# Kernel optimization log

Measured on AMD Instinct MI355X. Metric: run time of the kernel, lower is better.

## Reference

```python
import math
import jax, jax.numpy as jnp
import numpy as np

EPS = 1e-12
NHEAD = 12
HEAD_DIM = 64  # d_model // nhead = 768 // 12


def setup_inputs() -> dict:
    key = jax.random.key(0)
    ks = jax.random.split(key, 8)
    L, D, H = 12, 768, 2048
    B, S = 8, 1024
    std = 0.02
    return {
        "x": jax.random.normal(ks[0], (B, S, D), jnp.float32),
        "wq": jax.random.normal(ks[1], (L, D, D), jnp.float32) * std,
        "wk": jax.random.normal(ks[2], (L, D, D), jnp.float32) * std,
        "wv": jax.random.normal(ks[3], (L, D, D), jnp.float32) * std,
        "wo": jax.random.normal(ks[4], (L, D, D), jnp.float32) * std,
        "w1": jax.random.normal(ks[5], (L, H, D), jnp.float32) * std,
        "w2": jax.random.normal(ks[6], (L, D, H), jnp.float32) * std,
        "attn_norm_w": jnp.ones((L, D), jnp.float32),
        "ffn_norm_w": jnp.ones((L, D), jnp.float32),
    }


def _rmsnorm(x, w):
    # x * rsqrt(mean(x^2) + eps) * w
    return x * jax.lax.rsqrt(jnp.mean(x * x, axis=-1, keepdims=True) + EPS) * w


def _block(x, params):
    wq, wk, wv, wo, w1, w2, anw, fnw = params
    B, S, D = x.shape
    # --- attention (manual matmul-softmax-matmul, fp32 softmax) ---
    xn = _rmsnorm(x, anw)
    q = jnp.einsum('bsd,ed->bse', xn, wq).reshape(B, S, NHEAD, HEAD_DIM)
    k = jnp.einsum('bsd,ed->bse', xn, wk).reshape(B, S, NHEAD, HEAD_DIM)
    v = jnp.einsum('bsd,ed->bse', xn, wv).reshape(B, S, NHEAD, HEAD_DIM)
    scores = jnp.einsum('bqhd,bkhd->bhqk', q, k) / math.sqrt(HEAD_DIM)
    probs = jax.nn.softmax(scores.astype(jnp.float32), axis=-1).astype(x.dtype)
    attn = jnp.einsum('bhqk,bkhd->bqhd', probs, v).reshape(B, S, D)
    h = x + jnp.einsum('bsd,ed->bse', attn, wo)
    # --- FFN: w2(silu(w1(h_norm))) ---
    hn = _rmsnorm(h, fnw)
    ff = jnp.einsum('bsh,dh->bsd', jax.nn.silu(jnp.einsum('bsd,hd->bsh', hn, w1)), w2)
    return h + ff


def reference(x, wq, wk, wv, wo, w1, w2, attn_norm_w, ffn_norm_w):
    def step(carry, p):
        return _block(carry, p), None
    out, _ = jax.lax.scan(step, x, (wq, wk, wv, wo, w1, w2, attn_norm_w, ffn_norm_w))
    return out
```

## Files before the change

kernel.cpp:

```cpp
#include <hip/hip_runtime.h>
#include <stdint.h>

typedef unsigned short u16;
typedef unsigned int u32;
typedef __bf16 bf16x8 __attribute__((ext_vector_type(8)));
typedef __bf16 bf16x4 __attribute__((ext_vector_type(4)));
typedef float f32x4 __attribute__((ext_vector_type(4)));

__device__ __forceinline__ u16 f2bf(float f) {
  u32 u = __builtin_bit_cast(u32, f);
  u32 r = (u + 0x7FFFu + ((u >> 16) & 1u)) >> 16;
  return (u16)r;
}

__global__ __launch_bounds__(256)
void convert_w(const float* __restrict__ wq, const float* __restrict__ wk,
               const float* __restrict__ wv, const float* __restrict__ wo,
               const float* __restrict__ w1, const float* __restrict__ w2,
               u16* __restrict__ out) {
  size_t i = ((size_t)blockIdx.x * 256 + threadIdx.x) * 4;
  if (i >= 5505024) return;
  const float* src; size_t off;
  if (i < 589824)       { src = wq; off = i; }
  else if (i < 1179648) { src = wk; off = i - 589824; }
  else if (i < 1769472) { src = wv; off = i - 1179648; }
  else if (i < 2359296) { src = wo; off = i - 1769472; }
  else if (i < 3932160) { src = w1; off = i - 2359296; }
  else                  { src = w2; off = i - 3932160; }
  float4 v = *(const float4*)(src + off);
  u32 lo = (u32)f2bf(v.x) | ((u32)f2bf(v.y) << 16);
  u32 hi = (u32)f2bf(v.z) | ((u32)f2bf(v.w) << 16);
  *(uint2*)(out + i) = make_uint2(lo, hi);
}

__device__ __forceinline__ void rn_store4(u16* p, float4 v, float4 w, float sc) {
  u32 lo = (u32)f2bf(v.x * sc * w.x) | ((u32)f2bf(v.y * sc * w.y) << 16);
  u32 hi = (u32)f2bf(v.z * sc * w.z) | ((u32)f2bf(v.w * sc * w.w) << 16);
  *(uint2*)p = make_uint2(lo, hi);
}

__global__ __launch_bounds__(256)
void rmsnorm_k(const float* __restrict__ x, const float* __restrict__ w,
               u16* __restrict__ out) {
  const int tok = (blockIdx.x << 2) + (threadIdx.x >> 6);
  const int l = threadIdx.x & 63;
  const float* xr = x + (size_t)tok * 768;
  float4 v0 = *(const float4*)(xr + l * 4);
  float4 v1 = *(const float4*)(xr + 256 + l * 4);
  float4 v2 = *(const float4*)(xr + 512 + l * 4);
  float ss = v0.x*v0.x + v0.y*v0.y + v0.z*v0.z + v0.w*v0.w
           + v1.x*v1.x + v1.y*v1.y + v1.z*v1.z + v1.w*v1.w
           + v2.x*v2.x + v2.y*v2.y + v2.z*v2.z + v2.w*v2.w;
  ss += __shfl_xor(ss, 1);  ss += __shfl_xor(ss, 2);  ss += __shfl_xor(ss, 4);
  ss += __shfl_xor(ss, 8);  ss += __shfl_xor(ss, 16); ss += __shfl_xor(ss, 32);
  float sc = rsqrtf(ss * (1.f / 768.f) + 1e-12f);
  float4 w0 = *(const float4*)(w + l * 4);
  float4 w1v = *(const float4*)(w + 256 + l * 4);
  float4 w2v = *(const float4*)(w + 512 + l * 4);
  u16* o = out + (size_t)tok * 768;
  rn_store4(o + l * 4, v0, w0, sc);
  rn_store4(o + 256 + l * 4, v1, w1v, sc);
  rn_store4(o + 512 + l * 4, v2, w2v, sc);
}

#define GEMM_CORE(A_, W_, K_, m0_, n0_)                                             \
  for (int kt = 0; kt < (K_); kt += 64) {                                           \
    __syncthreads();                                                                \
    _Pragma("unroll")                                                               \
    for (int ii = 0; ii < 4; ++ii) {                                                \
      int issue = (w << 2) + ii;                                                    \
      int r = (issue << 3) + (l >> 3);                                              \
      int c = (l & 7) ^ (r & 7);                                                    \
      __builtin_amdgcn_global_load_lds((A_) + (size_t)((m0_) + r) * (K_) + kt + c * 8, \
                                       As + issue * 512, 16, 0, 0);                 \
      __builtin_amdgcn_global_load_lds((W_) + (size_t)((n0_) + r) * (K_) + kt + c * 8, \
                                       Ws + issue * 512, 16, 0, 0);                 \
    }                                                                               \
    __syncthreads();                                                                \
    _Pragma("unroll")                                                               \
    for (int kc = 0; kc < 2; ++kc) {                                                \
      int chunk = lg + (kc << 2);                                                   \
      bf16x8 af[4], bfr[4];                                                         \
      _Pragma("unroll")                                                             \
      for (int i = 0; i < 4; ++i) {                                                 \
        int mr = (wm << 6) + (i << 4) + ll;                                         \
        af[i] = *(const bf16x8*)((const char*)As + mr * 128 + ((chunk ^ (mr & 7)) << 4)); \
        int nr = (wn << 6) + (i << 4) + ll;                                         \
        bfr[i] = *(const bf16x8*)((const char*)Ws + nr * 128 + ((chunk ^ (nr & 7)) << 4)); \
      }                                                                             \
      _Pragma("unroll")                                                             \
      for (int i = 0; i < 4; ++i)                                                   \
        _Pragma("unroll")                                                           \
        for (int j = 0; j < 4; ++j)                                                 \
          acc[i][j] = __builtin_amdgcn_mfma_f32_16x16x32_bf16(af[i], bfr[j], acc[i][j], 0, 0, 0); \
    }                                                                               \
  }

template<int EP>
__global__ __launch_bounds__(256, 2)
void gemm_bt(const u16* __restrict__ A, const u16* __restrict__ W,
             void* __restrict__ outp, const float* __restrict__ Res,
             int M, int N, int K) {
  __shared__ __align__(16) u16 As[128 * 64];
  __shared__ __align__(16) u16 Ws[128 * 64];
  const int tid = threadIdx.x;
  const int w = tid >> 6, l = tid & 63;
  const int lg = l >> 4, ll = l & 15;
  const int ntiles = N >> 7;
  const int mt = blockIdx.x / ntiles, nt = blockIdx.x - mt * ntiles;
  const int m0 = mt << 7, n0 = nt << 7;
  const int wm = w >> 1, wn = w & 1;

  const f32x4 fz = {0.f, 0.f, 0.f, 0.f};
  f32x4 acc[4][4];
#pragma unroll
  for (int i = 0; i < 4; ++i)
#pragma unroll
    for (int j = 0; j < 4; ++j) acc[i][j] = fz;

  GEMM_CORE(A, W, K, m0, n0)

  const int g4 = lg << 2;
#pragma unroll
  for (int i = 0; i < 4; ++i) {
#pragma unroll
    for (int j = 0; j < 4; ++j) {
      int row0 = m0 + (wm << 6) + (i << 4) + g4;
      int col = n0 + (wn << 6) + (j << 4) + ll;
      f32x4 v = acc[i][j];
      if (EP == 0) {
        u16* o = (u16*)outp;
#pragma unroll
        for (int e = 0; e < 4; ++e) o[(size_t)(row0 + e) * N + col] = f2bf(v[e]);
      } else if (EP == 1) {
        float* o = (float*)outp;
#pragma unroll
        for (int e = 0; e < 4; ++e) {
          size_t idx = (size_t)(row0 + e) * N + col;
          o[idx] = Res[idx] + v[e];
        }
      } else {
        u16* o = (u16*)outp;
#pragma unroll
        for (int e = 0; e < 4; ++e) {
          float xx = v[e];
          o[(size_t)(row0 + e) * N + col] = f2bf(xx / (1.f + __expf(-xx)));
        }
      }
    }
  }
}

__global__ __launch_bounds__(256, 4)
void gemm_bt64(const u16* __restrict__ A, const u16* __restrict__ W,
               float* __restrict__ outp, const float* __restrict__ Res,
               int M, int N, int K) {
  __shared__ __align__(16) u16 As[64 * 64];
  __shared__ __align__(16) u16 Ws[128 * 64];
  const int tid = threadIdx.x;
  const int w = tid >> 6, l = tid & 63;
  const int lg = l >> 4, ll = l & 15;
  const int ntiles = N >> 7;
  const int mt = blockIdx.x / ntiles, nt = blockIdx.x - mt * ntiles;
  const int m0 = mt << 6, n0 = nt << 7;
  const int wm = w >> 1, wn = w & 1;

  const f32x4 fz = {0.f, 0.f, 0.f, 0.f};
  f32x4 acc[2][4];
#pragma unroll
  for (int i = 0; i < 2; ++i)
#pragma unroll
    for (int j = 0; j < 4; ++j) acc[i][j] = fz;

  for (int kt = 0; kt < K; kt += 64) {
    __syncthreads();
#pragma unroll
    for (int ii = 0; ii < 6; ++ii) {
      int issue = w * 6 + ii;
      if (issue < 8) {
        int r = (issue << 3) + (l >> 3);
        int c = (l & 7) ^ (r & 7);
        __builtin_amdgcn_global_load_lds(A + (size_t)(m0 + r) * K + kt + c * 8,
                                         As + issue * 512, 16, 0, 0);
      } else {
        int is2 = issue - 8;
        int r = (is2 << 3) + (l >> 3);
        int c = (l & 7) ^ (r & 7);
        __builtin_amdgcn_global_load_lds(W + (size_t)(n0 + r) * K + kt + c * 8,
                                         Ws + is2 * 512, 16, 0, 0);
      }
    }
    __syncthreads();
#pragma unroll
    for (int kc = 0; kc < 2; ++kc) {
      int chunk = lg + (kc << 2);
      bf16x8 af[2], bfr[4];
#pragma unroll
      for (int i = 0; i < 2; ++i) {
        int mr = (wm << 5) + (i << 4) + ll;
        af[i] = *(const bf16x8*)((const char*)As + mr * 128 + ((chunk ^ (mr & 7)) << 4));
      }
#pragma unroll
      for (int j = 0; j < 4; ++j) {
        int nr = (wn << 6) + (j << 4) + ll;
        bfr[j] = *(const bf16x8*)((const char*)Ws + nr * 128 + ((chunk ^ (nr & 7)) << 4));
      }
#pragma unroll
      for (int i = 0; i < 2; ++i)
#pragma unroll
        for (int j = 0; j < 4; ++j)
          acc[i][j] = __builtin_amdgcn_mfma_f32_16x16x32_bf16(af[i], bfr[j], acc[i][j], 0, 0, 0);
    }
  }

  const int g4 = lg << 2;
#pragma unroll
  for (int i = 0; i < 2; ++i) {
#pragma unroll
    for (int j = 0; j < 4; ++j) {
      int row0 = m0 + (wm << 5) + (i << 4) + g4;
      int col = n0 + (wn << 6) + (j << 4) + ll;
      f32x4 v = acc[i][j];
#pragma unroll
      for (int e = 0; e < 4; ++e) {
        size_t idx = (size_t)(row0 + e) * N + col;
        outp[idx] = Res[idx] + v[e];
      }
    }
  }
}

__global__ __launch_bounds__(256, 2)
void gemm_qkv(const u16* __restrict__ A, const u16* __restrict__ W,
              u16* __restrict__ Qo, u16* __restrict__ Ko, u16* __restrict__ Vo) {
  __shared__ __align__(16) u16 As[128 * 64];
  __shared__ __align__(16) u16 Ws[128 * 64];
  const int tid = threadIdx.x;
  const int w = tid >> 6, l = tid & 63;
  const int lg = l >> 4, ll = l & 15;
  const int mt = blockIdx.x / 18, nt = blockIdx.x - mt * 18;
  const int m0 = mt << 7, n0 = nt << 7;
  const int wm = w >> 1, wn = w & 1;
  const int K = 768;

  const f32x4 fz = {0.f, 0.f, 0.f, 0.f};
  f32x4 acc[4][4];
#pragma unroll
  for (int i = 0; i < 4; ++i)
#pragma unroll
    for (int j = 0; j < 4; ++j) acc[i][j] = fz;

  GEMM_CORE(A, W, K, m0, n0)

  const int g4 = lg << 2;
#pragma unroll
  for (int i = 0; i < 4; ++i) {
#pragma unroll
    for (int j = 0; j < 4; ++j) {
      int row0 = m0 + (wm << 6) + (i << 4) + g4;
      int col = n0 + (wn << 6) + (j << 4) + ll;
      f32x4 v = acc[i][j];
      if (nt < 12) {
        u16* o = (nt < 6) ? Qo : Ko;
        int c = (nt < 6) ? col : (col - 768);
#pragma unroll
        for (int e = 0; e < 4; ++e) o[(size_t)(row0 + e) * 768 + c] = f2bf(v[e]);
      } else {
        int c = col - 1536;
        int vrow = ((row0 >> 10) * 768) + c;
        u32 lo = (u32)f2bf(v[0]) | ((u32)f2bf(v[1]) << 16);
        u32 hi = (u32)f2bf(v[2]) | ((u32)f2bf(v[3]) << 16);
        *(uint2*)(Vo + ((size_t)vrow << 10) + (row0 & 1023)) = make_uint2(lo, hi);
      }
    }
  }
}

__global__ __launch_bounds__(256, 2)
void attn_kernel(const u16* __restrict__ Q, const u16* __restrict__ Kg,
                 const u16* __restrict__ Vt, u16* __restrict__ Og) {
  __shared__ __align__(16) __bf16 Ks[128 * 64];
  __shared__ __align__(16) __bf16 Vs[64 * 128];
  __shared__ __align__(16) __bf16 Ps[4][16 * 128];

  const int tid = threadIdx.x;
  const int w = tid >> 6, l = tid & 63;
  const int lg = l >> 4, ll = l & 15;
  const int bid = blockIdx.x;
  const int qt = bid / 96;
  const int bh = bid - qt * 96;
  const int b = bh / 12, hh = bh - b * 12;
  const float SC = 0.125f * 1.44269504f;

  bf16x8 qf[2][2];
  {
    const int tq = (b << 10) + (qt << 7) + (w << 5);
#pragma unroll
    for (int fm = 0; fm < 2; ++fm)
#pragma unroll
      for (int kc = 0; kc < 2; ++kc)
        qf[fm][kc] = *(const bf16x8*)(Q + (size_t)(tq + fm * 16 + ll) * 768 + hh * 64 + kc * 32 + lg * 8);
  }

  bf16x8 kp[4], vp[4];
#define ISSUE_KV(t_)                                                                  \
  { _Pragma("unroll")                                                                 \
    for (int ii = 0; ii < 4; ++ii) {                                                  \
      int issue = (w << 2) + ii;                                                      \
      int r = (issue << 3) + (l >> 3);                                                \
      int c = (l & 7) ^ (r & 7);                                                      \
      kp[ii] = *(const bf16x8*)(Kg + (size_t)((b << 10) + ((t_) << 7) + r) * 768 + hh * 64 + c * 8); \
      int rv = (issue << 2) + (l >> 4);                                               \
      int cv = ll ^ (rv & 7);                                                         \
      vp[ii] = *(const bf16x8*)(Vt + (size_t)((bh << 6) + rv) * 1024 + ((t_) << 7) + cv * 8); \
    } }
#define WRITE_KV                                                                      \
  { _Pragma("unroll")                                                                 \
    for (int ii = 0; ii < 4; ++ii) {                                                  \
      int issue = (w << 2) + ii;                                                      \
      *(bf16x8*)((char*)Ks + issue * 1024 + l * 16) = kp[ii];                         \
      *(bf16x8*)((char*)Vs + issue * 1024 + l * 16) = vp[ii];                         \
    } }

  const f32x4 fz = {0.f, 0.f, 0.f, 0.f};
  f32x4 oacc[4][2];
#pragma unroll
  for (int i = 0; i < 4; ++i) { oacc[i][0] = fz; oacc[i][1] = fz; }
  float mrow2[2] = {-1e30f, -1e30f};
  float lrow2[2] = {0.f, 0.f};

  ISSUE_KV(0);
  WRITE_KV;
  __syncthreads();

  for (int kt = 0; kt < 8; ++kt) {
    if (kt < 7) ISSUE_KV(kt + 1);

    f32x4 sa[2][8];
#pragma unroll
    for (int fm = 0; fm < 2; ++fm)
#pragma unroll
      for (int fn = 0; fn < 8; ++fn) sa[fm][fn] = fz;
    __builtin_amdgcn_s_setprio(1);
#pragma unroll
    for (int kc = 0; kc < 2; ++kc) {
      int chunk = lg + (kc << 2);
      bf16x8 kb[8];
#pragma unroll
      for (int fn = 0; fn < 8; ++fn) {
        int nr = (fn << 4) + ll;
        kb[fn] = *(const bf16x8*)((const char*)Ks + nr * 128 + ((chunk ^ (nr & 7)) << 4));
      }
#pragma unroll
      for (int fm = 0; fm < 2; ++fm)
#pragma unroll
        for (int fn = 0; fn < 8; ++fn)
          sa[fm][fn] = __builtin_amdgcn_mfma_f32_16x16x32_bf16(kb[fn], qf[fm][kc], sa[fm][fn], 0, 0, 0);
    }
    __builtin_amdgcn_s_setprio(0);

#pragma unroll
    for (int fm = 0; fm < 2; ++fm) {
      f32x4 vm = sa[fm][0];
#pragma unroll
      for (int fn = 1; fn < 8; ++fn) {
#pragma unroll
        for (int e = 0; e < 4; ++e) vm[e] = fmaxf(vm[e], sa[fm][fn][e]);
      }
      float mx = fmaxf(fmaxf(vm[0], vm[1]), fmaxf(vm[2], vm[3]));
      mx = fmaxf(mx, __shfl_xor(mx, 16));
      mx = fmaxf(mx, __shfl_xor(mx, 32));
      float mnew = fmaxf(mrow2[fm], mx);
      float c2 = mnew * SC;
      float scal = __builtin_amdgcn_exp2f(__builtin_fmaf(SC, mrow2[fm], -c2));

      f32x4 vsum = fz;
#pragma unroll
      for (int fn = 0; fn < 8; ++fn) {
        f32x4 p;
#pragma unroll
        for (int e = 0; e < 4; ++e)
          p[e] = __builtin_amdgcn_exp2f(__builtin_fmaf(SC, sa[fm][fn][e], -c2));
        vsum += p;
        bf16x4 pv4;
#pragma unroll
        for (int e = 0; e < 4; ++e) pv4[e] = (__bf16)p[e];
        int chunk = (fn << 1) + (lg >> 1);
        *(bf16x4*)((char*)&Ps[w][0] + ll * 256 + ((chunk ^ (ll & 7)) << 4) + ((lg & 1) << 3)) = pv4;
      }
      float rs = (vsum[0] + vsum[1]) + (vsum[2] + vsum[3]);
      rs += __shfl_xor(rs, 16);
      rs += __shfl_xor(rs, 32);
      lrow2[fm] = lrow2[fm] * scal + rs;
      mrow2[fm] = mnew;

      asm volatile("" ::: "memory");

#pragma unroll
      for (int fd = 0; fd < 4; ++fd) oacc[fd][fm] *= scal;

      __builtin_amdgcn_s_setprio(1);
#pragma unroll
      for (int ch = 0; ch < 4; ++ch) {
        int chunk = lg + (ch << 2);
        int qr = ll;
        bf16x8 pb = *(const bf16x8*)((const char*)&Ps[w][0] + qr * 256 + ((chunk ^ (qr & 7)) << 4));
#pragma unroll
        for (int fd = 0; fd < 4; ++fd) {
          int dr = (fd << 4) + ll;
          bf16x8 av = *(const bf16x8*)((const char*)Vs + dr * 256 + ((chunk ^ (dr & 7)) << 4));
          oacc[fd][fm] = __builtin_amdgcn_mfma_f32_16x16x32_bf16(av, pb, oacc[fd][fm], 0, 0, 0);
        }
      }
      __builtin_amdgcn_s_setprio(0);

      asm volatile("" ::: "memory");
    }

    if (kt < 7) {
      __syncthreads();
      WRITE_KV;
      __syncthreads();
    }
  }
#undef ISSUE_KV
#undef WRITE_KV

  float inv0 = 1.f / lrow2[0];
  float inv1 = 1.f / lrow2[1];
  const int tq0 = (b << 10) + (qt << 7) + (w << 5);
#pragma unroll
  for (int fd = 0; fd < 4; ++fd) {
#pragma unroll
    for (int fo = 0; fo < 2; ++fo) {
      int q = (fo << 4) + ll;
      float inv = fo ? inv1 : inv0;
      f32x4 v = oacc[fd][fo];
      int d0 = (fd << 4) + (lg << 2);
      u16* o = Og + (size_t)(tq0 + q) * 768 + hh * 64 + d0;
      u32 lo = (u32)f2bf(v[0] * inv) | ((u32)f2bf(v[1] * inv) << 16);
      u32 hi = (u32)f2bf(v[2] * inv) | ((u32)f2bf(v[3] * inv) << 16);
      *(uint2*)o = make_uint2(lo, hi);
    }
  }
}

extern "C" void kernel_launch(void* const* d_in, const int* in_sizes, int n_in,
                              void* d_out, int out_size, void* d_ws, size_t ws_size,
                              hipStream_t stream) {
  const float* x = (const float*)d_in[0];
  const float* wq = (const float*)d_in[1];
  const float* wk = (const float*)d_in[2];
  const float* wv = (const float*)d_in[3];
  const float* wo = (const float*)d_in[4];
  const float* w1 = (const float*)d_in[5];
  const float* w2 = (const float*)d_in[6];
  const float* anw = (const float*)d_in[7];
  const float* fnw = (const float*)d_in[8];

  char* ws = (char*)d_ws;
  float* h    = (float*)(ws);
  u16* xn     = (u16*)(ws + 25165824);
  u16* qb     = (u16*)(ws + 37748736);
  u16* kb     = (u16*)(ws + 50331648);
  u16* vt     = (u16*)(ws + 62914560);
  u16* ff1    = (u16*)(ws + 75497472);
  u16* wbuf   = (u16*)(ws + 109051904);

  hipMemcpyAsync(h, x, 25165824, hipMemcpyDeviceToDevice, stream);

  for (int L = 0; L < 12; ++L) {
    convert_w<<<5376, 256, 0, stream>>>(
        wq + (size_t)L * 589824, wk + (size_t)L * 589824,
        wv + (size_t)L * 589824, wo + (size_t)L * 589824,
        w1 + (size_t)L * 1572864, w2 + (size_t)L * 1572864, wbuf);
    rmsnorm_k<<<2048, 256, 0, stream>>>(h, anw + L * 768, xn);
    gemm_qkv<<<1152, 256, 0, stream>>>(xn, wbuf, qb, kb, vt);
    attn_kernel<<<768, 256, 0, stream>>>(qb, kb, vt, qb);
    gemm_bt64<<<768, 256, 0, stream>>>(qb, wbuf + 1769472, h, h, 8192, 768, 768);
    rmsnorm_k<<<2048, 256, 0, stream>>>(h, fnw + L * 768, xn);
    gemm_bt<2><<<1024, 256, 0, stream>>>(xn, wbuf + 2359296, ff1, nullptr, 8192, 2048, 768);
    float* outw = (L == 11) ? (float*)d_out : h;
    gemm_bt64<<<768, 256, 0, stream>>>(ff1, wbuf + 3932160, outw, h, 8192, 768, 2048);
  }
}
```

Measured before the change: 2.646 ms.

## Halve attention query tile per block and alias probability buffer onto K tile

The attention kernel now handles 64 query rows per block, 16 per wave, and launches twice as many blocks. The separate shared-memory buffer for softmax probabilities is removed; each wave writes its probabilities into its slice of the K tile, with an added barrier after the QK product. This cuts shared-memory use and per-thread registers, allowing more resident blocks and better latency hiding. In exchange, each K/V tile is fetched for half as many queries, doubling K/V global traffic, and one more barrier runs per key tile.

```diff
diff --git a/kernel.cpp b/kernel.cpp
--- a/kernel.cpp
+++ b/kernel.cpp
@@ -281,7 +281,6 @@
                  const u16* __restrict__ Vt, u16* __restrict__ Og) {
   __shared__ __align__(16) __bf16 Ks[128 * 64];
   __shared__ __align__(16) __bf16 Vs[64 * 128];
-  __shared__ __align__(16) __bf16 Ps[4][16 * 128];
 
   const int tid = threadIdx.x;
   const int w = tid >> 6, l = tid & 63;
@@ -292,15 +291,13 @@
   const int b = bh / 12, hh = bh - b * 12;
   const float SC = 0.125f * 1.44269504f;
 
-  bf16x8 qf[2][2];
-  {
-    const int tq = (b << 10) + (qt << 7) + (w << 5);
-#pragma unroll
-    for (int fm = 0; fm < 2; ++fm)
-#pragma unroll
-      for (int kc = 0; kc < 2; ++kc)
-        qf[fm][kc] = *(const bf16x8*)(Q + (size_t)(tq + fm * 16 + ll) * 768 + hh * 64 + kc * 32 + lg * 8);
-  }
+  __bf16* Pw = Ks + (w << 11);
+
+  bf16x8 qf[2];
+  const int tq0 = (b << 10) + (qt << 6) + (w << 4);
+#pragma unroll
+  for (int kc = 0; kc < 2; ++kc)
+    qf[kc] = *(const bf16x8*)(Q + (size_t)(tq0 + ll) * 768 + hh * 64 + kc * 32 + lg * 8);
 
   bf16x8 kp[4], vp[4];
 #define ISSUE_KV(t_)                                                                  \
@@ -323,11 +320,10 @@
     } }
 
   const f32x4 fz = {0.f, 0.f, 0.f, 0.f};
-  f32x4 oacc[4][2];
-#pragma unroll
-  for (int i = 0; i < 4; ++i) { oacc[i][0] = fz; oacc[i][1] = fz; }
-  float mrow2[2] = {-1e30f, -1e30f};
-  float lrow2[2] = {0.f, 0.f};
+  f32x4 oacc[4];
+#pragma unroll
+  for (int i = 0; i < 4; ++i) oacc[i] = fz;
+  float mrow = -1e30f, lrow = 0.f;
 
   ISSUE_KV(0);
   WRITE_KV;
@@ -336,11 +332,9 @@
   for (int kt = 0; kt < 8; ++kt) {
     if (kt < 7) ISSUE_KV(kt + 1);
 
-    f32x4 sa[2][8];
-#pragma unroll
-    for (int fm = 0; fm < 2; ++fm)
-#pragma unroll
-      for (int fn = 0; fn < 8; ++fn) sa[fm][fn] = fz;
+    f32x4 sa[8];
+#pragma unroll
+    for (int fn = 0; fn < 8; ++fn) sa[fn] = fz;
     __builtin_amdgcn_s_setprio(1);
 #pragma unroll
     for (int kc = 0; kc < 2; ++kc) {
@@ -352,70 +346,66 @@
         kb[fn] = *(const bf16x8*)((const char*)Ks + nr * 128 + ((chunk ^ (nr & 7)) << 4));
       }
 #pragma unroll
-      for (int fm = 0; fm < 2; ++fm)
-#pragma unroll
-        for (int fn = 0; fn < 8; ++fn)
-          sa[fm][fn] = __builtin_amdgcn_mfma_f32_16x16x32_bf16(kb[fn], qf[fm][kc], sa[fm][fn], 0, 0, 0);
+      for (int fn = 0; fn < 8; ++fn)
+        sa[fn] = __builtin_amdgcn_mfma_f32_16x16x32_bf16(kb[fn], qf[kc], sa[fn], 0, 0, 0);
     }
     __builtin_amdgcn_s_setprio(0);
 
-#pragma unroll
-    for (int fm = 0; fm < 2; ++fm) {
-      f32x4 vm = sa[fm][0];
-#pragma unroll
-      for (int fn = 1; fn < 8; ++fn) {
-#pragma unroll
-        for (int e = 0; e < 4; ++e) vm[e] = fmaxf(vm[e], sa[fm][fn][e]);
-      }
-      float mx = fmaxf(fmaxf(vm[0], vm[1]), fmaxf(vm[2], vm[3]));
-      mx = fmaxf(mx, __shfl_xor(mx, 16));
-      mx = fmaxf(mx, __shfl_xor(mx, 32));
-      float mnew = fmaxf(mrow2[fm], mx);
-      float c2 = mnew * SC;
-      float scal = __builtin_amdgcn_exp2f(__builtin_fmaf(SC, mrow2[fm], -c2));
-
-      f32x4 vsum = fz;
-#pragma unroll
-      for (int fn = 0; fn < 8; ++fn) {
-        f32x4 p;
-#pragma unroll
-        for (int e = 0; e < 4; ++e)
-          p[e] = __builtin_amdgcn_exp2f(__builtin_fmaf(SC, sa[fm][fn][e], -c2));
-        vsum += p;
-        bf16x4 pv4;
-#pragma unroll
-        for (int e = 0; e < 4; ++e) pv4[e] = (__bf16)p[e];
-        int chunk = (fn << 1) + (lg >> 1);
-        *(bf16x4*)((char*)&Ps[w][0] + ll * 256 + ((chunk ^ (ll & 7)) << 4) + ((lg & 1) << 3)) = pv4;
-      }
-      float rs = (vsum[0] + vsum[1]) + (vsum[2] + vsum[3]);
-      rs += __shfl_xor(rs, 16);
-      rs += __shfl_xor(rs, 32);
-      lrow2[fm] = lrow2[fm] * scal + rs;
-      mrow2[fm] = mnew;
-
-      asm volatile("" ::: "memory");
-
-#pragma unroll
-      for (int fd = 0; fd < 4; ++fd) oacc[fd][fm] *= scal;
-
-      __builtin_amdgcn_s_setprio(1);
-#pragma unroll
-      for (int ch = 0; ch < 4; ++ch) {
-        int chunk = lg + (ch << 2);
-        int qr = ll;
-        bf16x8 pb = *(const bf16x8*)((const char*)&Ps[w][0] + qr * 256 + ((chunk ^ (qr & 7)) << 4));
-#pragma unroll
-        for (int fd = 0; fd < 4; ++fd) {
-          int dr = (fd << 4) + ll;
-          bf16x8 av = *(const bf16x8*)((const char*)Vs + dr * 256 + ((chunk ^ (dr & 7)) << 4));
-          oacc[fd][fm] = __builtin_amdgcn_mfma_f32_16x16x32_bf16(av, pb, oacc[fd][fm], 0, 0, 0);
-        }
-      }
-      __builtin_amdgcn_s_setprio(0);
-
-      asm volatile("" ::: "memory");
-    }
+    __syncthreads();
+
+    f32x4 vm = sa[0];
+#pragma unroll
+    for (int fn = 1; fn < 8; ++fn) {
+#pragma unroll
+      for (int e = 0; e < 4; ++e) vm[e] = fmaxf(vm[e], sa[fn][e]);
+    }
+    float mx = fmaxf(fmaxf(vm[0], vm[1]), fmaxf(vm[2], vm[3]));
+    mx = fmaxf(mx, __shfl_xor(mx, 16));
+    mx = fmaxf(mx, __shfl_xor(mx, 32));
+    float mnew = fmaxf(mrow, mx);
+    float c2 = mnew * SC;
+    float scal = __builtin_amdgcn_exp2f(__builtin_fmaf(SC, mrow, -c2));
+
+    f32x4 vsum = fz;
+#pragma unroll
+    for (int fn = 0; fn < 8; ++fn) {
+      f32x4 p;
+#pragma unroll
+      for (int e = 0; e < 4; ++e)
+        p[e] = __builtin_amdgcn_exp2f(__builtin_fmaf(SC, sa[fn][e], -c2));
+      vsum += p;
+      bf16x4 pv4;
+#pragma unroll
+      for (int e = 0; e < 4; ++e) pv4[e] = (__bf16)p[e];
+      int chunk = (fn << 1) + (lg >> 1);
+      *(bf16x4*)((char*)Pw + ll * 256 + ((chunk ^ (ll & 7)) << 4) + ((lg & 1) << 3)) = pv4;
+    }
+    float rs = (vsum[0] + vsum[1]) + (vsum[2] + vsum[3]);
+    rs += __shfl_xor(rs, 16);
+    rs += __shfl_xor(rs, 32);
+    lrow = lrow * scal + rs;
+    mrow = mnew;
+
+    asm volatile("" ::: "memory");
+
+#pragma unroll
+    for (int fd = 0; fd < 4; ++fd) oacc[fd] *= scal;
+
+    __builtin_amdgcn_s_setprio(1);
+#pragma unroll
+    for (int ch = 0; ch < 4; ++ch) {
+      int chunk = lg + (ch << 2);
+      bf16x8 pb = *(const bf16x8*)((const char*)Pw + ll * 256 + ((chunk ^ (ll & 7)) << 4));
+#pragma unroll
+      for (int fd = 0; fd < 4; ++fd) {
+        int dr = (fd << 4) + ll;
+        bf16x8 av = *(const bf16x8*)((const char*)Vs + dr * 256 + ((chunk ^ (dr & 7)) << 4));
+        oacc[fd] = __builtin_amdgcn_mfma_f32_16x16x32_bf16(av, pb, oacc[fd], 0, 0, 0);
+      }
+    }
+    __builtin_amdgcn_s_setprio(0);
+
+    asm volatile("" ::: "memory");
 
     if (kt < 7) {
       __syncthreads();
@@ -426,22 +416,15 @@
 #undef ISSUE_KV
 #undef WRITE_KV
 
-  float inv0 = 1.f / lrow2[0];
-  float inv1 = 1.f / lrow2[1];
-  const int tq0 = (b << 10) + (qt << 7) + (w << 5);
+  float inv = 1.f / lrow;
 #pragma unroll
   for (int fd = 0; fd < 4; ++fd) {
-#pragma unroll
-    for (int fo = 0; fo < 2; ++fo) {
-      int q = (fo << 4) + ll;
-      float inv = fo ? inv1 : inv0;
-      f32x4 v = oacc[fd][fo];
-      int d0 = (fd << 4) + (lg << 2);
-      u16* o = Og + (size_t)(tq0 + q) * 768 + hh * 64 + d0;
-      u32 lo = (u32)f2bf(v[0] * inv) | ((u32)f2bf(v[1] * inv) << 16);
-      u32 hi = (u32)f2bf(v[2] * inv) | ((u32)f2bf(v[3] * inv) << 16);
-      *(uint2*)o = make_uint2(lo, hi);
-    }
+    f32x4 v = oacc[fd];
+    int d0 = (fd << 4) + (lg << 2);
+    u16* o = Og + (size_t)(tq0 + ll) * 768 + hh * 64 + d0;
+    u32 lo = (u32)f2bf(v[0] * inv) | ((u32)f2bf(v[1] * inv) << 16);
+    u32 hi = (u32)f2bf(v[2] * inv) | ((u32)f2bf(v[3] * inv) << 16);
+    *(uint2*)o = make_uint2(lo, hi);
   }
 }
 
@@ -476,7 +459,7 @@
         w1 + (size_t)L * 1572864, w2 + (size_t)L * 1572864, wbuf);
     rmsnorm_k<<<2048, 256, 0, stream>>>(h, anw + L * 768, xn);
     gemm_qkv<<<1152, 256, 0, stream>>>(xn, wbuf, qb, kb, vt);
-    attn_kernel<<<768, 256, 0, stream>>>(qb, kb, vt, qb);
+    attn_kernel<<<1536, 256, 0, stream>>>(qb, kb, vt, qb);
     gemm_bt64<<<768, 256, 0, stream>>>(qb, wbuf + 1769472, h, h, 8192, 768, 768);
     rmsnorm_k<<<2048, 256, 0, stream>>>(h, fnw + L * 768, xn);
     gemm_bt<2><<<1024, 256, 0, stream>>>(xn, wbuf + 2359296, ff1, nullptr, 8192, 2048, 768);
```

Measured after the change: 2.647 ms. About the same (+0.0%).
